# Optimization experiments

Hardware: AMD Instinct MI355X
Metric: run time of the kernel (lower is better)

## Reference

```python
import jax, jax.numpy as jnp
import numpy as np

VEC, H, B, S = 768, 256, 64, 512


def setup_inputs() -> dict:
    key = jax.random.key(0)
    ks = jax.random.split(key, 8)
    sc = 0.02
    return {
        "output_1": jax.random.normal(ks[0], (B, S, VEC), dtype=jnp.float32),
        "output_2": jax.random.normal(ks[1], (B, S, VEC), dtype=jnp.float32),
        "mlp_w": jax.random.normal(ks[2], (H, VEC), dtype=jnp.float32) * sc,
        "mlp_b": jnp.zeros((H,), dtype=jnp.float32),
        "fd_w": jax.random.normal(ks[3], (H, 2 * H), dtype=jnp.float32) * sc,
        "fd_b": jnp.zeros((H,), dtype=jnp.float32),
        "ff_w": jax.random.normal(ks[4], (1, H), dtype=jnp.float32) * sc,
        "ff_b": jnp.zeros((1,), dtype=jnp.float32),
    }


def reference(output_1, output_2, mlp_w, mlp_b, fd_w, fd_b, ff_w, ff_b):
    # eval-mode forward of Bert_coss
    o1 = jax.nn.relu(output_1 @ mlp_w.T + mlp_b)        # [B,S,H]
    o2 = jax.nn.relu(output_2 @ mlp_w.T + mlp_b)        # [B,S,H]
    o1_doc = jnp.mean(o1, axis=1)                        # [B,H]
    o2_doc = jnp.mean(o2, axis=1)                        # [B,H]
    h = jax.nn.relu(jnp.concatenate([o1_doc, o2_doc], axis=1) @ fd_w.T + fd_b)
    out = jax.nn.sigmoid(jnp.squeeze(h @ ff_w.T + ff_b))  # [B]
    # append doc vectors as an extra token
    o1e = jnp.concatenate([o1, o1_doc[:, None, :]], axis=1)  # [B,S+1,H]
    o2e = jnp.concatenate([o2, o2_doc[:, None, :]], axis=1)  # [B,S+1,H]
    # graph_match: scores + softmax over dim=1; only last column is used downstream
    a = jnp.einsum('bsh,bth->bst', o1e, o2e)             # [B,S+1,S+1]
    a_x = jax.nn.softmax(a, axis=1)
    att = a_x[:, :, -1].T                                # [S+1,B]
    att = jnp.concatenate([att[:-1], out[None, :]], axis=0)  # [S+1,B]
    return att
```

## Files before the change

### kernel.cpp

```cpp
#include <hip/hip_runtime.h>
#include <hip/hip_bf16.h>
#include <math.h>

#define B_ 64
#define S_ 512
#define VEC_ 768
#define H_ 256
#define M_ (B_*S_)

typedef float floatx4 __attribute__((ext_vector_type(4)));
typedef __bf16 bf16x8 __attribute__((ext_vector_type(8)));
typedef __bf16 bf16x4 __attribute__((ext_vector_type(4)));

__global__ __launch_bounds__(256) void prep_kernel(
    const float* __restrict__ mlp_w, __bf16* __restrict__ wbf, float* __restrict__ sums)
{
  const int bid = blockIdx.x;
  if (bid < 192) {
    const int i = bid * 256 + threadIdx.x;
    const float4 v = ((const float4*)mlp_w)[i];
    bf16x4 b = { (__bf16)v.x, (__bf16)v.y, (__bf16)v.z, (__bf16)v.w };
    *(bf16x4*)&wbf[(size_t)i * 4] = b;
  } else {
    const int i = (bid - 192) * 256 + threadIdx.x;
    ((float4*)sums)[i] = make_float4(0.f, 0.f, 0.f, 0.f);
  }
}

#define ABUF_ 16384
#define BUFB_ 24576
#define LDSB_ 49152

__device__ __forceinline__ void gl_lds16(char* l, const void* g) {
  __builtin_amdgcn_global_load_lds(
      (const __attribute__((address_space(1))) unsigned int*)g,
      (__attribute__((address_space(3))) unsigned int*)l, 16, 0, 0);
}

#define STAGE(bufbase, kk)                                                    \
  {                                                                           \
    _Pragma("unroll")                                                         \
    for (int i_ = 0; i_ < 4; i_++) {                \
      const int ch = t + i_ * 256;                                            \
      const int row = ch >> 3;                                                \
      const int cc = (ch & 7) ^ (row & 7);     \
      gl_lds16(smem + (bufbase) + ch * 16,                                    \
               Abase + (size_t)row * VEC_ + (kk) + cc * 4);                   \
    }                                                                         \
    _Pragma("unroll")                                                         \
    for (int i_ = 0; i_ < 2; i_++) {                 \
      const int ch = t + i_ * 256;                                            \
      const int row = ch >> 2;                                                \
      const int cc = ((ch & 3) ^ row ^ (row >> 2)) & 3;                       \
      gl_lds16(smem + (bufbase) + ABUF_ + ch * 16,                            \
               Bbase + (size_t)row * VEC_ + (kk) + cc * 8);                   \
    }                                                                         \
  }

#define COMPUTE(bufbase)                                                      \
  {                                                                           \
    const char* Ab = smem + (bufbase);                                        \
    const char* Bb = smem + (bufbase) + ABUF_;                                \
    bf16x8 af[4]; bf16x8 bfr[4];                                              \
    _Pragma("unroll")                                                         \
    for (int i = 0; i < 4; i++) {                                             \
      const int base = (wm + i * 16 + c) * 128;                               \
      const floatx4 a0 = *(const floatx4*)(Ab + base + aslot0);               \
      const floatx4 a1 = *(const floatx4*)(Ab + base + (aslot0 ^ 16));        \
      bf16x8 v;                                                               \
      v[0] = (__bf16)a0[0]; v[1] = (__bf16)a0[1];                             \
      v[2] = (__bf16)a0[2]; v[3] = (__bf16)a0[3];                             \
      v[4] = (__bf16)a1[0]; v[5] = (__bf16)a1[1];                             \
      v[6] = (__bf16)a1[2]; v[7] = (__bf16)a1[3];                             \
      af[i] = v;                                                              \
    }                                                                         \
    _Pragma("unroll")                                                         \
    for (int j = 0; j < 4; j++)                                               \
      bfr[j] = *(const bf16x8*)(Bb + (wn + j * 16 + c) * 64 + bslot);         \
    _Pragma("unroll")                                                         \
    for (int i = 0; i < 4; i++)                                               \
      _Pragma("unroll")                                                       \
      for (int j = 0; j < 4; j++)                                             \
        acc[i][j] = __builtin_amdgcn_mfma_f32_16x16x32_bf16(af[i], bfr[j],    \
                                                            acc[i][j], 0, 0, 0); \
  }

__global__ __launch_bounds__(256, 3) void gemm_doc_kernel(
    const float* __restrict__ out1, const float* __restrict__ out2,
    const __bf16* __restrict__ wbf, const float* __restrict__ mlp_b,
    __bf16* __restrict__ o1, float* __restrict__ sum1, float* __restrict__ sum2)
{
  __shared__ __align__(16) char smem[LDSB_];

  const int tensor = blockIdx.z;
  const float* __restrict__ A = tensor ? out2 : out1;
  float* __restrict__ dsum = tensor ? sum2 : sum1;

  const int n0 = blockIdx.x * 128;
  const int m0 = blockIdx.y * 128;
  const int bidx = m0 >> 9;

  const int t = threadIdx.x;
  const int lane = t & 63;
  const int wave = t >> 6;
  const int q = lane >> 4;
  const int c = lane & 15;
  const int wm = (wave >> 1) * 64;
  const int wn = (wave & 1) * 64;

  const int aslot0 = (((2 * q) ^ (c & 7)) << 4);
  const int bslot  = (((q ^ c ^ (c >> 2)) & 3) << 4);

  const float* Abase = &A[(size_t)m0 * VEC_];
  const __bf16* Bbase = &wbf[(size_t)n0 * VEC_];

  floatx4 acc[4][4];
#pragma unroll
  for (int i = 0; i < 4; i++)
#pragma unroll
    for (int j = 0; j < 4; j++)
      acc[i][j] = (floatx4){0.f, 0.f, 0.f, 0.f};

  STAGE(0, 0);
  __syncthreads();

  int bufb = 0;
  int kk = 32;
#pragma unroll 1
  for (int kt = 0; kt < 23; ++kt) {
    STAGE(bufb ^ BUFB_, kk);
    COMPUTE(bufb);
    kk += 32;
    __syncthreads();
    bufb ^= BUFB_;
  }
  COMPUTE(bufb);

#pragma unroll
  for (int j = 0; j < 4; j++) {
    const int n = n0 + wn + j * 16 + c;
    const float bias = mlp_b[n];
    float colsum = 0.f;
#pragma unroll
    for (int i = 0; i < 4; i++) {
      const int mbase = m0 + wm + i * 16 + q * 4;
#pragma unroll
      for (int r = 0; r < 4; r++) {
        float v = acc[i][j][r] + bias;
        v = fmaxf(v, 0.f);
        colsum += v;
        if (tensor == 0) o1[(size_t)(mbase + r) * H_ + n] = (__bf16)v;
      }
    }
    colsum += __shfl_down(colsum, 32);
    colsum += __shfl_down(colsum, 16);
    if (lane < 16)
      atomicAdd(&dsum[bidx * H_ + n0 + wn + j * 16 + lane], colsum);
  }
}

__global__ __launch_bounds__(256) void logits_kernel(
    const __bf16* __restrict__ o1, const float* __restrict__ sum1,
    const float* __restrict__ sum2, float* __restrict__ lg)
{
  const int b = blockIdx.y;
  const int t = threadIdx.x, lane = t & 63, wave = t >> 6;
  const int s = blockIdx.x * 4 + wave;
  if (s > 512) return;
  const float sc = 1.f / 512.f;
  const float4 w4 = ((const float4*)&sum2[b * H_])[lane];
  float p;
  if (s < 512) {
    const bf16x4 x = ((const bf16x4*)&o1[((size_t)b * S_ + s) * H_])[lane];
    p = ((float)x[0] * w4.x + (float)x[1] * w4.y +
         (float)x[2] * w4.z + (float)x[3] * w4.w) * sc;
  } else {
    const float4 x = ((const float4*)&sum1[b * H_])[lane];
    p = (x.x * w4.x + x.y * w4.y + x.z * w4.z + x.w * w4.w) * sc * sc;
  }
  p += __shfl_down(p, 32); p += __shfl_down(p, 16); p += __shfl_down(p, 8);
  p += __shfl_down(p, 4);  p += __shfl_down(p, 2);  p += __shfl_down(p, 1);
  if (lane == 0) lg[b * 513 + s] = p;
}

__global__ __launch_bounds__(256) void softmax_head_kernel(
    const float* __restrict__ lg, const float* __restrict__ sum1, const float* __restrict__ sum2,
    const float* __restrict__ fd_w, const float* __restrict__ fd_b,
    const float* __restrict__ ff_w, const float* __restrict__ ff_b,
    float* __restrict__ out)
{
  const int b = blockIdx.x, t = threadIdx.x, lane = t & 63, wave = t >> 6;
  __shared__ __align__(16) float dc[512];
  __shared__ float sl[513];
  __shared__ float red[4], r1[4], r2[4];

  dc[t]       = sum1[b * H_ + t] * (1.f / 512.f);
  dc[t + 256] = sum2[b * H_ + t] * (1.f / 512.f);
  for (int i = t; i < 513; i += 256) sl[i] = lg[b * 513 + i];
  __syncthreads();
  const float4* wrow = (const float4*)&fd_w[(size_t)t * 512];
  const float4* dc4  = (const float4*)dc;
  float a0 = 0.f, a1 = 0.f;
#pragma unroll 8
  for (int k = 0; k < 128; k += 2) {
    const float4 w0 = wrow[k],     d0 = dc4[k];
    const float4 w1 = wrow[k + 1], d1 = dc4[k + 1];
    a0 += w0.x * d0.x + w0.y * d0.y + w0.z * d0.z + w0.w * d0.w;
    a1 += w1.x * d1.x + w1.y * d1.y + w1.z * d1.z + w1.w * d1.w;
  }
  const float h = fmaxf(a0 + a1 + fd_b[t], 0.f);
  float part = ff_w[t] * h;
  part += __shfl_down(part, 32); part += __shfl_down(part, 16);
  part += __shfl_down(part, 8);  part += __shfl_down(part, 4);
  part += __shfl_down(part, 2);  part += __shfl_down(part, 1);
  if (lane == 0) red[wave] = part;

  float m = -1e30f;
  for (int i = t; i < 513; i += 256) m = fmaxf(m, sl[i]);
  m = fmaxf(m, __shfl_down(m, 32)); m = fmaxf(m, __shfl_down(m, 16));
  m = fmaxf(m, __shfl_down(m, 8));  m = fmaxf(m, __shfl_down(m, 4));
  m = fmaxf(m, __shfl_down(m, 2));  m = fmaxf(m, __shfl_down(m, 1));
  if (lane == 0) r1[wave] = m;
  __syncthreads();
  m = fmaxf(fmaxf(r1[0], r1[1]), fmaxf(r1[2], r1[3]));
  float psum = 0.f;
  for (int i = t; i < 513; i += 256) { const float e = expf(sl[i] - m); sl[i] = e; psum += e; }
  psum += __shfl_down(psum, 32); psum += __shfl_down(psum, 16); psum += __shfl_down(psum, 8);
  psum += __shfl_down(psum, 4);  psum += __shfl_down(psum, 2);  psum += __shfl_down(psum, 1);
  if (lane == 0) r2[wave] = psum;
  __syncthreads();
  const float inv = 1.f / (r2[0] + r2[1] + r2[2] + r2[3]);
  for (int s = t; s < 512; s += 256) out[s * 64 + b] = sl[s] * inv;
  if (t == 0) {
    const float tot = red[0] + red[1] + red[2] + red[3] + ff_b[0];
    out[(size_t)512 * 64 + b] = 1.f / (1.f + expf(-tot));
  }
}

extern "C" void kernel_launch(void* const* d_in, const int* in_sizes, int n_in,
                              void* d_out, int out_size, void* d_ws, size_t ws_size,
                              hipStream_t stream) {
  const float* out1  = (const float*)d_in[0];
  const float* out2  = (const float*)d_in[1];
  const float* mlp_w = (const float*)d_in[2];
  const float* mlp_b = (const float*)d_in[3];
  const float* fd_w  = (const float*)d_in[4];
  const float* fd_b  = (const float*)d_in[5];
  const float* ff_w  = (const float*)d_in[6];
  const float* ff_b  = (const float*)d_in[7];
  float* out = (float*)d_out;

  __bf16* o1  = (__bf16*)d_ws;
  __bf16* wbf = o1 + (size_t)M_ * H_;
  float*  s1  = (float*)(wbf + (size_t)H_ * VEC_);
  float*  s2  = s1 + B_ * H_;
  float*  lgw = s2 + B_ * H_;

  prep_kernel<<<224, 256, 0, stream>>>(mlp_w, wbf, s1);
  gemm_doc_kernel<<<dim3(2, 256, 2), 256, 0, stream>>>(out1, out2, wbf, mlp_b, o1, s1, s2);
  logits_kernel<<<dim3(129, B_), 256, 0, stream>>>(o1, s1, s2, lgw);
  softmax_head_kernel<<<B_, 256, 0, stream>>>(lgw, s1, s2, fd_w, fd_b, ff_w, ff_b, out);
}
```

Before: 293.9 us.

## Stage GEMM tiles through registers with bf16 conversion before LDS write

Replaces the direct global-to-LDS loads of fp32 A tiles with register-prefetched loads two k-steps ahead. A is converted to bf16 before being stored into LDS, so both A and B tiles use a compact 64-byte-row swizzled layout and the LDS buffer size drops. The loop is restructured into ping-pong STEP macros with one barrier per step, and launch bounds move from 3 to 2 blocks per CU. The aim is to cut LDS traffic and per-MFMA conversion work, at the cost of more registers and lower occupancy.

```diff
diff --git a/kernel.cpp b/kernel.cpp
--- a/kernel.cpp
+++ b/kernel.cpp
@@ -27,56 +27,37 @@
   }
 }
 
-#define ABUF_ 16384
-#define BUFB_ 24576
-#define LDSB_ 49152
-
-__device__ __forceinline__ void gl_lds16(char* l, const void* g) {
-  __builtin_amdgcn_global_load_lds(
-      (const __attribute__((address_space(1))) unsigned int*)g,
-      (__attribute__((address_space(3))) unsigned int*)l, 16, 0, 0);
-}
-
-#define STAGE(bufbase, kk)                                                    \
+#define BUFSZ_ 16384
+#define LDSB_  32768
+
+__device__ __forceinline__ bf16x8 cvt8(float4 a, float4 b) {
+  bf16x8 v;
+  v[0] = (__bf16)a.x; v[1] = (__bf16)a.y; v[2] = (__bf16)a.z; v[3] = (__bf16)a.w;
+  v[4] = (__bf16)b.x; v[5] = (__bf16)b.y; v[6] = (__bf16)b.z; v[7] = (__bf16)b.w;
+  return v;
+}
+
+#define LOADT(A0, A1, A2, A3, Bv0, Bv1, kk)                                   \
   {                                                                           \
-    _Pragma("unroll")                                                         \
-    for (int i_ = 0; i_ < 4; i_++) {                \
-      const int ch = t + i_ * 256;                                            \
-      const int row = ch >> 3;                                                \
-      const int cc = (ch & 7) ^ (row & 7);     \
-      gl_lds16(smem + (bufbase) + ch * 16,                                    \
-               Abase + (size_t)row * VEC_ + (kk) + cc * 4);                   \
-    }                                                                         \
-    _Pragma("unroll")                                                         \
-    for (int i_ = 0; i_ < 2; i_++) {                 \
-      const int ch = t + i_ * 256;                                            \
-      const int row = ch >> 2;                                                \
-      const int cc = ((ch & 3) ^ row ^ (row >> 2)) & 3;                       \
-      gl_lds16(smem + (bufbase) + ABUF_ + ch * 16,                            \
-               Bbase + (size_t)row * VEC_ + (kk) + cc * 8);                   \
-    }                                                                         \
+    const float*  pA_ = Aload + (kk);                                         \
+    const __bf16* pB_ = Bload + (kk);                                         \
+    A0 = *(const float4*)pA_;                                                 \
+    A1 = *(const float4*)(pA_ + 4);                                           \
+    A2 = *(const float4*)(pA_ + 64 * VEC_);                                   \
+    A3 = *(const float4*)(pA_ + 64 * VEC_ + 4);                               \
+    Bv0 = *(const bf16x8*)pB_;                                                \
+    Bv1 = *(const bf16x8*)(pB_ + 64 * VEC_);                                  \
   }
 
 #define COMPUTE(bufbase)                                                      \
   {                                                                           \
-    const char* Ab = smem + (bufbase);                                        \
-    const char* Bb = smem + (bufbase) + ABUF_;                                \
-    bf16x8 af[4]; bf16x8 bfr[4];                                              \
+    bf16x8 af[4], bfr[4];                                                     \
     _Pragma("unroll")                                                         \
-    for (int i = 0; i < 4; i++) {                                             \
-      const int base = (wm + i * 16 + c) * 128;                               \
-      const floatx4 a0 = *(const floatx4*)(Ab + base + aslot0);               \
-      const floatx4 a1 = *(const floatx4*)(Ab + base + (aslot0 ^ 16));        \
-      bf16x8 v;                                                               \
-      v[0] = (__bf16)a0[0]; v[1] = (__bf16)a0[1];                             \
-      v[2] = (__bf16)a0[2]; v[3] = (__bf16)a0[3];                             \
-      v[4] = (__bf16)a1[0]; v[5] = (__bf16)a1[1];                             \
-      v[6] = (__bf16)a1[2]; v[7] = (__bf16)a1[3];                             \
-      af[i] = v;                                                              \
-    }                                                                         \
+    for (int i = 0; i < 4; i++)                                               \
+      af[i] = *(const bf16x8*)(smem + (bufbase) + (wm + i * 16 + c) * 64 + aslot); \
     _Pragma("unroll")                                                         \
     for (int j = 0; j < 4; j++)                                               \
-      bfr[j] = *(const bf16x8*)(Bb + (wn + j * 16 + c) * 64 + bslot);         \
+      bfr[j] = *(const bf16x8*)(smem + (bufbase) + 8192 + (wn + j * 16 + c) * 64 + aslot); \
     _Pragma("unroll")                                                         \
     for (int i = 0; i < 4; i++)                                               \
       _Pragma("unroll")                                                       \
@@ -85,7 +66,19 @@
                                                             acc[i][j], 0, 0, 0); \
   }
 
-__global__ __launch_bounds__(256, 3) void gemm_doc_kernel(
+#define STEP(A0, A1, A2, A3, Bv0, Bv1, bufbase, kk2, DOLOAD)                  \
+  {                                                                           \
+    *(bf16x8*)(smem + (bufbase) + woff)               = cvt8(A0, A1);         \
+    *(bf16x8*)(smem + (bufbase) + woff + 4096)        = cvt8(A2, A3);         \
+    *(bf16x8*)(smem + (bufbase) + 8192 + woff)        = Bv0;                  \
+    *(bf16x8*)(smem + (bufbase) + 8192 + woff + 4096) = Bv1;                  \
+    if (DOLOAD) { LOADT(A0, A1, A2, A3, Bv0, Bv1, kk2) }                      \
+    asm volatile("s_waitcnt lgkmcnt(0)" ::: "memory");                        \
+    __builtin_amdgcn_s_barrier();                                             \
+    COMPUTE(bufbase);                                                         \
+  }
+
+__global__ __launch_bounds__(256, 2) void gemm_doc_kernel(
     const float* __restrict__ out1, const float* __restrict__ out2,
     const __bf16* __restrict__ wbf, const float* __restrict__ mlp_b,
     __bf16* __restrict__ o1, float* __restrict__ sum1, float* __restrict__ sum2)
@@ -108,11 +101,12 @@
   const int wm = (wave >> 1) * 64;
   const int wn = (wave & 1) * 64;
 
-  const int aslot0 = (((2 * q) ^ (c & 7)) << 4);
-  const int bslot  = (((q ^ c ^ (c >> 2)) & 3) << 4);
-
-  const float* Abase = &A[(size_t)m0 * VEC_];
-  const __bf16* Bbase = &wbf[(size_t)n0 * VEC_];
+  const int srow = t >> 2;
+  const int woff = srow * 64 + ((((t & 3) ^ (srow & 3) ^ ((srow >> 2) & 3))) << 4);
+  const float*  Aload = A   + (size_t)(m0 + srow) * VEC_ + (t & 3) * 8;
+  const __bf16* Bload = wbf + (size_t)(n0 + srow) * VEC_ + (t & 3) * 8;
+
+  const int aslot = ((q ^ (c & 3) ^ (c >> 2)) << 4);
 
   floatx4 acc[4][4];
 #pragma unroll
@@ -121,20 +115,18 @@
     for (int j = 0; j < 4; j++)
       acc[i][j] = (floatx4){0.f, 0.f, 0.f, 0.f};
 
-  STAGE(0, 0);
-  __syncthreads();
-
-  int bufb = 0;
-  int kk = 32;
+  float4 a0, a1, a2, a3, e0, e1, e2, e3;
+  bf16x8 b0, b1, f0, f1;
+  LOADT(a0, a1, a2, a3, b0, b1, 0)
+  LOADT(e0, e1, e2, e3, f0, f1, 32)
+
 #pragma unroll 1
-  for (int kt = 0; kt < 23; ++kt) {
-    STAGE(bufb ^ BUFB_, kk);
-    COMPUTE(bufb);
-    kk += 32;
-    __syncthreads();
-    bufb ^= BUFB_;
-  }
-  COMPUTE(bufb);
+  for (int it = 0; it < 11; ++it) {
+    STEP(a0, a1, a2, a3, b0, b1, 0,      (2 * it + 2) * 32, 1)
+    STEP(e0, e1, e2, e3, f0, f1, BUFSZ_, (2 * it + 3) * 32, 1)
+  }
+  STEP(a0, a1, a2, a3, b0, b1, 0,      0, 0)
+  STEP(e0, e1, e2, e3, f0, f1, BUFSZ_, 0, 0)
 
 #pragma unroll
   for (int j = 0; j < 4; j++) {
```

New measurement: 292.1 us. No clear change (-0.6%).
